# Kernel optimization log

Hardware: AMD Instinct MI355X
Metric: run time of the kernel (lower is better)

The kernel has to match this reference:

```python
import jax, jax.numpy as jnp
import numpy as np

N_NODES = 100000
N_EDGES = 1200000
D_IN = 64
D_HID = 64


def setup_inputs() -> dict:
    key = jax.random.key(0)
    k1, k2, k3, k4 = jax.random.split(key, 4)
    x = jax.random.normal(k1, (N_NODES, D_IN), dtype=jnp.float32)
    edge_index = jax.random.randint(k2, (2, N_EDGES), 0, N_NODES, dtype=jnp.int32)
    edge_attr = jax.random.uniform(k3, (N_EDGES,), dtype=jnp.float32)
    W = jax.random.normal(k4, (D_HID, D_IN), dtype=jnp.float32) / np.sqrt(D_IN)
    b = jnp.zeros((D_HID,), dtype=jnp.float32)
    return {"x": x, "edge_index": edge_index, "edge_attr": edge_attr, "W": W, "b": b}


def _gcn_conv(x, edge_index, edge_weight, W, b):
    # PyG GCNConv: add self-loops (weight 1), symmetric normalization,
    # linear transform, scatter-add aggregation at target (col), bias.
    n = x.shape[0]
    loop = jnp.arange(n, dtype=edge_index.dtype)
    row = jnp.concatenate([edge_index[0], loop])  # source
    col = jnp.concatenate([edge_index[1], loop])  # target
    ew = jnp.concatenate([edge_weight, jnp.ones((n,), edge_weight.dtype)])
    deg = jax.ops.segment_sum(ew, col, num_segments=n)  # [N]
    dis = jnp.where(deg > 0, jax.lax.rsqrt(deg), 0.0)
    norm = dis[row] * ew * dis[col]                     # [E+N]
    h = x @ W.T                                          # [N, D_HID]
    msg = norm[:, None] * h[row]                         # [E+N, D_HID]
    out = jax.ops.segment_sum(msg, col, num_segments=n)  # [N, D_HID]
    return out + b


def reference(x, edge_index, edge_attr, W, b):
    # layer_num=2 -> single GCNConv; dropout is identity in eval mode.
    h = _gcn_conv(x, edge_index, edge_attr, W, b)
    return jax.nn.relu(h)
```

## Files before the change

kernel.cpp:

```cpp
#include <hip/hip_runtime.h>

#define N_NODES 100000
#define N_EDGES 1200000
#define D 64
#define KP 68
#define TN 64
#define CAP 48
#define Q15 32767.0f
#define INVQ15 (1.0f / 32767.0f)
#define BW 512
#define BSH 9
#define NBKT ((N_NODES + BW - 1) / BW)
#define CAPB 8192

__device__ __forceinline__ unsigned short f2bf(float f) {
    unsigned u = __float_as_uint(f);
    return (unsigned short)((u + 0x7FFFu + ((u >> 16) & 1u)) >> 16);
}
__device__ __forceinline__ float bf2f(unsigned short h) {
    return __uint_as_float((unsigned)h << 16);
}

__global__ __launch_bounds__(256) void k_coarse(const int4* __restrict__ row4,
                                                const int4* __restrict__ col4,
                                                const float4* __restrict__ ew4,
                                                int* __restrict__ gcur,
                                                int2* __restrict__ coarse, int n4) {
    __shared__ int lcnt[NBKT];
    __shared__ int lbase[NBKT];
    int t = threadIdx.x;
    for (int i = t; i < NBKT; i += 256) lcnt[i] = 0;
    __syncthreads();

    int bkt[8]; int slot[8]; int2 rec[8];
    #pragma unroll
    for (int k = 0; k < 8; k++) bkt[k] = -1;

    #pragma unroll
    for (int r = 0; r < 2; r++) {
        int q = blockIdx.x * 512 + r * 256 + t;
        if (q < n4) {
            int4 rr = row4[q]; int4 cc = col4[q]; float4 ww = ew4[q];
            int j = r * 4;
            int c;
            c = cc.x; bkt[j+0] = c >> BSH;
            rec[j+0] = make_int2(rr.x, ((c & (BW-1)) << 15) | (int)(ww.x * Q15 + 0.5f));
            slot[j+0] = atomicAdd(&lcnt[bkt[j+0]], 1);
            c = cc.y; bkt[j+1] = c >> BSH;
            rec[j+1] = make_int2(rr.y, ((c & (BW-1)) << 15) | (int)(ww.y * Q15 + 0.5f));
            slot[j+1] = atomicAdd(&lcnt[bkt[j+1]], 1);
            c = cc.z; bkt[j+2] = c >> BSH;
            rec[j+2] = make_int2(rr.z, ((c & (BW-1)) << 15) | (int)(ww.z * Q15 + 0.5f));
            slot[j+2] = atomicAdd(&lcnt[bkt[j+2]], 1);
            c = cc.w; bkt[j+3] = c >> BSH;
            rec[j+3] = make_int2(rr.w, ((c & (BW-1)) << 15) | (int)(ww.w * Q15 + 0.5f));
            slot[j+3] = atomicAdd(&lcnt[bkt[j+3]], 1);
        }
    }
    __syncthreads();
    for (int i = t; i < NBKT; i += 256) lbase[i] = atomicAdd(&gcur[i], lcnt[i]);
    __syncthreads();
    #pragma unroll
    for (int k = 0; k < 8; k++) {
        if (bkt[k] >= 0) {
            int pos = lbase[bkt[k]] + slot[k];
            if (pos < CAPB) coarse[(size_t)bkt[k] * CAPB + pos] = rec[k];
        }
    }
}

__global__ __launch_bounds__(256) void k_bin(const int* __restrict__ gcur,
                                             const int2* __restrict__ coarse,
                                             int* __restrict__ cnt,
                                             float* __restrict__ dis,
                                             unsigned int* __restrict__ em, int n_nodes) {
    __shared__ int   cur512[BW];
    __shared__ float d512[BW];
    int b = blockIdx.x, t = threadIdx.x;
    int total = min(gcur[b], CAPB);
    int nbase = b * BW;
    int bw = min(BW, n_nodes - nbase);
    for (int i = t; i < BW; i += 256) { cur512[i] = 0; d512[i] = 0.f; }
    __syncthreads();
    const int2* src = &coarse[(size_t)b * CAPB];
    for (int i = t; i < total; i += 256) {
        int2 r = src[i];
        int cl = (r.y >> 15) & (BW - 1);
        float w = (float)(r.y & 0x7FFF) * INVQ15;
        int s = atomicAdd(&cur512[cl], 1);
        atomicAdd(&d512[cl], w);
        if (s < CAP)
            em[(size_t)(nbase + cl) * CAP + s] = ((unsigned)r.x << 15) | (unsigned)(r.y & 0x7FFF);
    }
    __syncthreads();
    for (int i = t; i < bw; i += 256) {
        cnt[nbase + i] = cur512[i];
        dis[nbase + i] = rsqrtf(1.0f + d512[i]);
    }
}

__global__ __launch_bounds__(256) void k_agg_cap(const int* __restrict__ cnt,
                                                 const unsigned int* __restrict__ em,
                                                 const unsigned short* __restrict__ hsb,
                                                 const float* __restrict__ dis,
                                                 const float* __restrict__ b,
                                                 float* __restrict__ out, int n_nodes) {
    int w = threadIdx.x >> 6, l = threadIdx.x & 63;
    int n = blockIdx.x * 4 + w;
    if (n >= n_nodes) return;
    int c = min(cnt[n], CAP);
    int recs = (int)em[(size_t)n * CAP + min(l, CAP - 1)];
    float acc = bf2f(hsb[(size_t)n * D + l]);

    int i = 0;
    for (; i + 8 <= c; i += 8) {
        unsigned r0 = (unsigned)__shfl(recs, i + 0);
        unsigned r1 = (unsigned)__shfl(recs, i + 1);
        unsigned r2 = (unsigned)__shfl(recs, i + 2);
        unsigned r3 = (unsigned)__shfl(recs, i + 3);
        unsigned r4 = (unsigned)__shfl(recs, i + 4);
        unsigned r5 = (unsigned)__shfl(recs, i + 5);
        unsigned r6 = (unsigned)__shfl(recs, i + 6);
        unsigned r7 = (unsigned)__shfl(recs, i + 7);
        float h0 = bf2f(hsb[(size_t)(r0 >> 15) * D + l]);
        float h1 = bf2f(hsb[(size_t)(r1 >> 15) * D + l]);
        float h2 = bf2f(hsb[(size_t)(r2 >> 15) * D + l]);
        float h3 = bf2f(hsb[(size_t)(r3 >> 15) * D + l]);
        float h4 = bf2f(hsb[(size_t)(r4 >> 15) * D + l]);
        float h5 = bf2f(hsb[(size_t)(r5 >> 15) * D + l]);
        float h6 = bf2f(hsb[(size_t)(r6 >> 15) * D + l]);
        float h7 = bf2f(hsb[(size_t)(r7 >> 15) * D + l]);
        acc = fmaf((float)(r0 & 0x7FFFu) * INVQ15, h0, acc);
        acc = fmaf((float)(r1 & 0x7FFFu) * INVQ15, h1, acc);
        acc = fmaf((float)(r2 & 0x7FFFu) * INVQ15, h2, acc);
        acc = fmaf((float)(r3 & 0x7FFFu) * INVQ15, h3, acc);
        acc = fmaf((float)(r4 & 0x7FFFu) * INVQ15, h4, acc);
        acc = fmaf((float)(r5 & 0x7FFFu) * INVQ15, h5, acc);
        acc = fmaf((float)(r6 & 0x7FFFu) * INVQ15, h6, acc);
        acc = fmaf((float)(r7 & 0x7FFFu) * INVQ15, h7, acc);
    }
    for (; i + 4 <= c; i += 4) {
        unsigned r0 = (unsigned)__shfl(recs, i + 0);
        unsigned r1 = (unsigned)__shfl(recs, i + 1);
        unsigned r2 = (unsigned)__shfl(recs, i + 2);
        unsigned r3 = (unsigned)__shfl(recs, i + 3);
        float h0 = bf2f(hsb[(size_t)(r0 >> 15) * D + l]);
        float h1 = bf2f(hsb[(size_t)(r1 >> 15) * D + l]);
        float h2 = bf2f(hsb[(size_t)(r2 >> 15) * D + l]);
        float h3 = bf2f(hsb[(size_t)(r3 >> 15) * D + l]);
        acc = fmaf((float)(r0 & 0x7FFFu) * INVQ15, h0, acc);
        acc = fmaf((float)(r1 & 0x7FFFu) * INVQ15, h1, acc);
        acc = fmaf((float)(r2 & 0x7FFFu) * INVQ15, h2, acc);
        acc = fmaf((float)(r3 & 0x7FFFu) * INVQ15, h3, acc);
    }
    for (; i < c; i++) {
        unsigned r = (unsigned)__shfl(recs, i);
        acc = fmaf((float)(r & 0x7FFFu) * INVQ15, bf2f(hsb[(size_t)(r >> 15) * D + l]), acc);
    }
    float v = fmaf(dis[n], acc, b[l]);
    out[(size_t)n * D + l] = v > 0.f ? v : 0.f;
}

__global__ __launch_bounds__(256) void k_gemm_tile(const float* __restrict__ x,
                                                   const float* __restrict__ W,
                                                   const float* __restrict__ dis,
                                                   unsigned short* __restrict__ hsb, int n_nodes) {
    __shared__ float wt[D * KP];
    int t = threadIdx.x;
    int base = blockIdx.x * TN;
    #pragma unroll
    for (int c = 0; c < 16; c++) {
        int idx = t + c * 256;
        wt[(idx & 63) * KP + (idx >> 6)] = W[idx];
    }
    __syncthreads();

    int tx = t & 15, ty = t >> 4;
    int f0 = tx * 4, n0 = base + ty * 4;
    const float* xr0 = x + (size_t)min(n0 + 0, n_nodes - 1) * D;
    const float* xr1 = x + (size_t)min(n0 + 1, n_nodes - 1) * D;
    const float* xr2 = x + (size_t)min(n0 + 2, n_nodes - 1) * D;
    const float* xr3 = x + (size_t)min(n0 + 3, n_nodes - 1) * D;

    float acc[4][4] = {};
    #pragma unroll 4
    for (int k = 0; k < D; k += 4) {
        float a[4][4], wv[4][4];
        *(float4*)a[0] = *(const float4*)&xr0[k];
        *(float4*)a[1] = *(const float4*)&xr1[k];
        *(float4*)a[2] = *(const float4*)&xr2[k];
        *(float4*)a[3] = *(const float4*)&xr3[k];
        #pragma unroll
        for (int kk = 0; kk < 4; kk++)
            *(float4*)wv[kk] = *(const float4*)&wt[(k + kk) * KP + f0];
        #pragma unroll
        for (int kk = 0; kk < 4; kk++)
            #pragma unroll
            for (int j = 0; j < 4; j++)
                #pragma unroll
                for (int ff = 0; ff < 4; ff++)
                    acc[j][ff] = fmaf(a[j][kk], wv[kk][ff], acc[j][ff]);
    }
    #pragma unroll
    for (int j = 0; j < 4; j++) {
        int n = n0 + j;
        if (n < n_nodes) {
            float dv = dis[n];
            unsigned short h0 = f2bf(dv * acc[j][0]);
            unsigned short h1 = f2bf(dv * acc[j][1]);
            unsigned short h2 = f2bf(dv * acc[j][2]);
            unsigned short h3 = f2bf(dv * acc[j][3]);
            uint2 pk;
            pk.x = (unsigned)h0 | ((unsigned)h1 << 16);
            pk.y = (unsigned)h2 | ((unsigned)h3 << 16);
            *(uint2*)&hsb[(size_t)n * D + f0] = pk;
        }
    }
}

extern "C" void kernel_launch(void* const* d_in, const int* in_sizes, int n_in,
                              void* d_out, int out_size, void* d_ws, size_t ws_size,
                              hipStream_t stream) {
    const float* x   = (const float*)d_in[0];
    const int*   ei  = (const int*)d_in[1];
    const float* ew  = (const float*)d_in[2];
    const float* W   = (const float*)d_in[3];
    const float* b   = (const float*)d_in[4];
    float* out = (float*)d_out;

    const int* row = ei;
    const int* col = ei + N_EDGES;

    char* p = (char*)d_ws;
    auto carve = [&](size_t bytes) { char* q = p; p += (bytes + 255) & ~(size_t)255; return q; };
    float*          dis    = (float*)carve(N_NODES * sizeof(float));
    unsigned short* hsb    = (unsigned short*)carve((size_t)N_NODES * D * sizeof(unsigned short));
    int*            cnt    = (int*)  carve(N_NODES * sizeof(int));
    unsigned int*   em     = (unsigned int*)carve((size_t)N_NODES * CAP * sizeof(unsigned int));
    int*            gcur   = (int*)  carve(NBKT * sizeof(int));
    int2*           coarse = (int2*) carve((size_t)NBKT * CAPB * sizeof(int2));

    hipMemsetAsync(gcur, 0, NBKT * sizeof(int), stream);

    int n4 = N_EDGES / 4;
    int nbA = (n4 + 511) / 512;
    k_coarse<<<nbA, 256, 0, stream>>>(
        (const int4*)row, (const int4*)col, (const float4*)ew, gcur, coarse, n4);
    k_bin<<<NBKT, 256, 0, stream>>>(gcur, coarse, cnt, dis, em, N_NODES);
    k_gemm_tile<<<(N_NODES + TN - 1) / TN, 256, 0, stream>>>(x, W, dis, hsb, N_NODES);
    k_agg_cap<<<(N_NODES + 3) / 4, 256, 0, stream>>>(cnt, em, hsb, dis, b, out, N_NODES);
}
```

Before: 172.4 us.

## Replace two-pass bucketed binning with direct packed 64-bit global atomics

Drops the coarse bucketing kernel and the per-bucket binning kernel. Each edge now does one 64-bit global atomicAdd on a per-node word that packs the slot count in the high bits and a fixed-point weight sum in the low bits, then writes its record straight into the target node's capped slot list. The degree normalisation is folded into the GEMM epilogue. This saves a launch and the coarse buffer round trip, at the cost of 1.2M scattered global atomics and scattered 4-byte stores instead of shared-memory atomics.

```diff
diff --git a/kernel.cpp b/kernel.cpp
--- a/kernel.cpp
+++ b/kernel.cpp
@@ -8,10 +8,9 @@
 #define CAP 48
 #define Q15 32767.0f
 #define INVQ15 (1.0f / 32767.0f)
-#define BW 512
-#define BSH 9
-#define NBKT ((N_NODES + BW - 1) / BW)
-#define CAPB 8192
+#define Q28 268435456.0f
+#define INVQ28 3.7252902984619140625e-09f
+#define CD_MASK ((1ULL << 40) - 1)
 
 __device__ __forceinline__ unsigned short f2bf(float f) {
     unsigned u = __float_as_uint(f);
@@ -21,85 +20,32 @@
     return __uint_as_float((unsigned)h << 16);
 }
 
-__global__ __launch_bounds__(256) void k_coarse(const int4* __restrict__ row4,
+__global__ __launch_bounds__(256) void k_direct(const int4* __restrict__ row4,
                                                 const int4* __restrict__ col4,
                                                 const float4* __restrict__ ew4,
-                                                int* __restrict__ gcur,
-                                                int2* __restrict__ coarse, int n4) {
-    __shared__ int lcnt[NBKT];
-    __shared__ int lbase[NBKT];
-    int t = threadIdx.x;
-    for (int i = t; i < NBKT; i += 256) lcnt[i] = 0;
-    __syncthreads();
+                                                unsigned long long* __restrict__ cd,
+                                                unsigned int* __restrict__ em, int n4) {
+    int q = blockIdx.x * 256 + threadIdx.x;
+    if (q >= n4) return;
+    int4 rr = row4[q];
+    int4 cc = col4[q];
+    float4 ww = ew4[q];
 
-    int bkt[8]; int slot[8]; int2 rec[8];
-    #pragma unroll
-    for (int k = 0; k < 8; k++) bkt[k] = -1;
-
-    #pragma unroll
-    for (int r = 0; r < 2; r++) {
-        int q = blockIdx.x * 512 + r * 256 + t;
-        if (q < n4) {
-            int4 rr = row4[q]; int4 cc = col4[q]; float4 ww = ew4[q];
-            int j = r * 4;
-            int c;
-            c = cc.x; bkt[j+0] = c >> BSH;
-            rec[j+0] = make_int2(rr.x, ((c & (BW-1)) << 15) | (int)(ww.x * Q15 + 0.5f));
-            slot[j+0] = atomicAdd(&lcnt[bkt[j+0]], 1);
-            c = cc.y; bkt[j+1] = c >> BSH;
-            rec[j+1] = make_int2(rr.y, ((c & (BW-1)) << 15) | (int)(ww.y * Q15 + 0.5f));
-            slot[j+1] = atomicAdd(&lcnt[bkt[j+1]], 1);
-            c = cc.z; bkt[j+2] = c >> BSH;
-            rec[j+2] = make_int2(rr.z, ((c & (BW-1)) << 15) | (int)(ww.z * Q15 + 0.5f));
-            slot[j+2] = atomicAdd(&lcnt[bkt[j+2]], 1);
-            c = cc.w; bkt[j+3] = c >> BSH;
-            rec[j+3] = make_int2(rr.w, ((c & (BW-1)) << 15) | (int)(ww.w * Q15 + 0.5f));
-            slot[j+3] = atomicAdd(&lcnt[bkt[j+3]], 1);
-        }
-    }
-    __syncthreads();
-    for (int i = t; i < NBKT; i += 256) lbase[i] = atomicAdd(&gcur[i], lcnt[i]);
-    __syncthreads();
-    #pragma unroll
-    for (int k = 0; k < 8; k++) {
-        if (bkt[k] >= 0) {
-            int pos = lbase[bkt[k]] + slot[k];
-            if (pos < CAPB) coarse[(size_t)bkt[k] * CAPB + pos] = rec[k];
-        }
-    }
+    unsigned long long o0 = atomicAdd(&cd[cc.x], (1ULL << 40) | (unsigned long long)(ww.x * Q28));
+    unsigned long long o1 = atomicAdd(&cd[cc.y], (1ULL << 40) | (unsigned long long)(ww.y * Q28));
+    unsigned long long o2 = atomicAdd(&cd[cc.z], (1ULL << 40) | (unsigned long long)(ww.z * Q28));
+    unsigned long long o3 = atomicAdd(&cd[cc.w], (1ULL << 40) | (unsigned long long)(ww.w * Q28));
+    int s0 = (int)(o0 >> 40);
+    int s1 = (int)(o1 >> 40);
+    int s2 = (int)(o2 >> 40);
+    int s3 = (int)(o3 >> 40);
+    if (s0 < CAP) em[(size_t)cc.x * CAP + s0] = ((unsigned)rr.x << 15) | (unsigned)(int)(ww.x * Q15 + 0.5f);
+    if (s1 < CAP) em[(size_t)cc.y * CAP + s1] = ((unsigned)rr.y << 15) | (unsigned)(int)(ww.y * Q15 + 0.5f);
+    if (s2 < CAP) em[(size_t)cc.z * CAP + s2] = ((unsigned)rr.z << 15) | (unsigned)(int)(ww.z * Q15 + 0.5f);
+    if (s3 < CAP) em[(size_t)cc.w * CAP + s3] = ((unsigned)rr.w << 15) | (unsigned)(int)(ww.w * Q15 + 0.5f);
 }
 
-__global__ __launch_bounds__(256) void k_bin(const int* __restrict__ gcur,
-                                             const int2* __restrict__ coarse,
-                                             int* __restrict__ cnt,
-                                             float* __restrict__ dis,
-                                             unsigned int* __restrict__ em, int n_nodes) {
-    __shared__ int   cur512[BW];
-    __shared__ float d512[BW];
-    int b = blockIdx.x, t = threadIdx.x;
-    int total = min(gcur[b], CAPB);
-    int nbase = b * BW;
-    int bw = min(BW, n_nodes - nbase);
-    for (int i = t; i < BW; i += 256) { cur512[i] = 0; d512[i] = 0.f; }
-    __syncthreads();
-    const int2* src = &coarse[(size_t)b * CAPB];
-    for (int i = t; i < total; i += 256) {
-        int2 r = src[i];
-        int cl = (r.y >> 15) & (BW - 1);
-        float w = (float)(r.y & 0x7FFF) * INVQ15;
-        int s = atomicAdd(&cur512[cl], 1);
-        atomicAdd(&d512[cl], w);
-        if (s < CAP)
-            em[(size_t)(nbase + cl) * CAP + s] = ((unsigned)r.x << 15) | (unsigned)(r.y & 0x7FFF);
-    }
-    __syncthreads();
-    for (int i = t; i < bw; i += 256) {
-        cnt[nbase + i] = cur512[i];
-        dis[nbase + i] = rsqrtf(1.0f + d512[i]);
-    }
-}
-
-__global__ __launch_bounds__(256) void k_agg_cap(const int* __restrict__ cnt,
+__global__ __launch_bounds__(256) void k_agg_cap(const unsigned long long* __restrict__ cd,
                                                  const unsigned int* __restrict__ em,
                                                  const unsigned short* __restrict__ hsb,
                                                  const float* __restrict__ dis,
@@ -108,7 +54,7 @@
     int w = threadIdx.x >> 6, l = threadIdx.x & 63;
     int n = blockIdx.x * 4 + w;
     if (n >= n_nodes) return;
-    int c = min(cnt[n], CAP);
+    int c = min((int)(cd[n] >> 40), CAP);
     int recs = (int)em[(size_t)n * CAP + min(l, CAP - 1)];
     float acc = bf2f(hsb[(size_t)n * D + l]);
 
@@ -163,7 +109,8 @@
 
 __global__ __launch_bounds__(256) void k_gemm_tile(const float* __restrict__ x,
                                                    const float* __restrict__ W,
-                                                   const float* __restrict__ dis,
+                                                   const unsigned long long* __restrict__ cd,
+                                                   float* __restrict__ dis,
                                                    unsigned short* __restrict__ hsb, int n_nodes) {
     __shared__ float wt[D * KP];
     int t = threadIdx.x;
@@ -205,7 +152,9 @@
     for (int j = 0; j < 4; j++) {
         int n = n0 + j;
         if (n < n_nodes) {
-            float dv = dis[n];
+            float wsum = (float)(cd[n] & CD_MASK) * INVQ28;
+            float dv = rsqrtf(1.0f + wsum);
+            dis[n] = dv;
             unsigned short h0 = f2bf(dv * acc[j][0]);
             unsigned short h1 = f2bf(dv * acc[j][1]);
             unsigned short h2 = f2bf(dv * acc[j][2]);
@@ -233,20 +182,17 @@
 
     char* p = (char*)d_ws;
     auto carve = [&](size_t bytes) { char* q = p; p += (bytes + 255) & ~(size_t)255; return q; };
-    float*          dis    = (float*)carve(N_NODES * sizeof(float));
-    unsigned short* hsb    = (unsigned short*)carve((size_t)N_NODES * D * sizeof(unsigned short));
-    int*            cnt    = (int*)  carve(N_NODES * sizeof(int));
-    unsigned int*   em     = (unsigned int*)carve((size_t)N_NODES * CAP * sizeof(unsigned int));
-    int*            gcur   = (int*)  carve(NBKT * sizeof(int));
-    int2*           coarse = (int2*) carve((size_t)NBKT * CAPB * sizeof(int2));
+    float*              dis = (float*)carve(N_NODES * sizeof(float));
+    unsigned short*     hsb = (unsigned short*)carve((size_t)N_NODES * D * sizeof(unsigned short));
+    unsigned long long* cd  = (unsigned long long*)carve(N_NODES * sizeof(unsigned long long));
+    unsigned int*       em  = (unsigned int*)carve((size_t)N_NODES * CAP * sizeof(unsigned int));
 
-    hipMemsetAsync(gcur, 0, NBKT * sizeof(int), stream);
+    hipMemsetAsync(cd, 0, N_NODES * sizeof(unsigned long long), stream);
 
     int n4 = N_EDGES / 4;
-    int nbA = (n4 + 511) / 512;
-    k_coarse<<<nbA, 256, 0, stream>>>(
-        (const int4*)row, (const int4*)col, (const float4*)ew, gcur, coarse, n4);
-    k_bin<<<NBKT, 256, 0, stream>>>(gcur, coarse, cnt, dis, em, N_NODES);
-    k_gemm_tile<<<(N_NODES + TN - 1) / TN, 256, 0, stream>>>(x, W, dis, hsb, N_NODES);
-    k_agg_cap<<<(N_NODES + 3) / 4, 256, 0, stream>>>(cnt, em, hsb, dis, b, out, N_NODES);
+    int nbA = (n4 + 255) / 256;
+    k_direct<<<nbA, 256, 0, stream>>>(
+        (const int4*)row, (const int4*)col, (const float4*)ew, cd, em, n4);
+    k_gemm_tile<<<(N_NODES + TN - 1) / TN, 256, 0, stream>>>(x, W, cd, dis, hsb, N_NODES);
+    k_agg_cap<<<(N_NODES + 3) / 4, 256, 0, stream>>>(cd, em, hsb, dis, b, out, N_NODES);
 }
```

New measurement: 234.9 us. 36.3% more time.

## Process two nodes per wavefront in aggregation, widen bin blocks, skip empty atomics

Applied to the files above, without the earlier changes.

The aggregation kernel now has each wavefront handle two destination nodes and interleave their 4-wide gather loops, so more independent gathers are in flight per wave. The binning kernel launches with 512 threads instead of 256 to work through each bucket faster. The coarse pass skips the global atomic for buckets with zero local count. The aggregation drops its bounds check and relies on the node count being divisible by 8. It also loses the 8-wide unroll, which may lower per-wave memory parallelism when degrees are uneven.

```diff
diff --git a/kernel.cpp b/kernel.cpp
--- a/kernel.cpp
+++ b/kernel.cpp
@@ -58,7 +58,10 @@
         }
     }
     __syncthreads();
-    for (int i = t; i < NBKT; i += 256) lbase[i] = atomicAdd(&gcur[i], lcnt[i]);
+    for (int i = t; i < NBKT; i += 256) {
+        int c = lcnt[i];
+        lbase[i] = c ? atomicAdd(&gcur[i], c) : 0;
+    }
     __syncthreads();
     #pragma unroll
     for (int k = 0; k < 8; k++) {
@@ -69,7 +72,7 @@
     }
 }
 
-__global__ __launch_bounds__(256) void k_bin(const int* __restrict__ gcur,
+__global__ __launch_bounds__(512) void k_bin(const int* __restrict__ gcur,
                                              const int2* __restrict__ coarse,
                                              int* __restrict__ cnt,
                                              float* __restrict__ dis,
@@ -80,10 +83,10 @@
     int total = min(gcur[b], CAPB);
     int nbase = b * BW;
     int bw = min(BW, n_nodes - nbase);
-    for (int i = t; i < BW; i += 256) { cur512[i] = 0; d512[i] = 0.f; }
+    for (int i = t; i < BW; i += 512) { cur512[i] = 0; d512[i] = 0.f; }
     __syncthreads();
     const int2* src = &coarse[(size_t)b * CAPB];
-    for (int i = t; i < total; i += 256) {
+    for (int i = t; i < total; i += 512) {
         int2 r = src[i];
         int cl = (r.y >> 15) & (BW - 1);
         float w = (float)(r.y & 0x7FFF) * INVQ15;
@@ -93,12 +96,17 @@
             em[(size_t)(nbase + cl) * CAP + s] = ((unsigned)r.x << 15) | (unsigned)(r.y & 0x7FFF);
     }
     __syncthreads();
-    for (int i = t; i < bw; i += 256) {
+    for (int i = t; i < bw; i += 512) {
         cnt[nbase + i] = cur512[i];
         dis[nbase + i] = rsqrtf(1.0f + d512[i]);
     }
 }
 
+#define AGG_STEP(rec, accv)                                                          \
+    {                                                                                \
+        float hh = bf2f(hsb[(size_t)((rec) >> 15) * D + l]);                         \
+        accv = fmaf((float)((rec) & 0x7FFFu) * INVQ15, hh, accv);                    \
+    }
 __global__ __launch_bounds__(256) void k_agg_cap(const int* __restrict__ cnt,
                                                  const unsigned int* __restrict__ em,
                                                  const unsigned short* __restrict__ hsb,
@@ -106,59 +114,85 @@
                                                  const float* __restrict__ b,
                                                  float* __restrict__ out, int n_nodes) {
     int w = threadIdx.x >> 6, l = threadIdx.x & 63;
-    int n = blockIdx.x * 4 + w;
-    if (n >= n_nodes) return;
-    int c = min(cnt[n], CAP);
-    int recs = (int)em[(size_t)n * CAP + min(l, CAP - 1)];
-    float acc = bf2f(hsb[(size_t)n * D + l]);
-
-    int i = 0;
-    for (; i + 8 <= c; i += 8) {
-        unsigned r0 = (unsigned)__shfl(recs, i + 0);
-        unsigned r1 = (unsigned)__shfl(recs, i + 1);
-        unsigned r2 = (unsigned)__shfl(recs, i + 2);
-        unsigned r3 = (unsigned)__shfl(recs, i + 3);
-        unsigned r4 = (unsigned)__shfl(recs, i + 4);
-        unsigned r5 = (unsigned)__shfl(recs, i + 5);
-        unsigned r6 = (unsigned)__shfl(recs, i + 6);
-        unsigned r7 = (unsigned)__shfl(recs, i + 7);
-        float h0 = bf2f(hsb[(size_t)(r0 >> 15) * D + l]);
-        float h1 = bf2f(hsb[(size_t)(r1 >> 15) * D + l]);
-        float h2 = bf2f(hsb[(size_t)(r2 >> 15) * D + l]);
-        float h3 = bf2f(hsb[(size_t)(r3 >> 15) * D + l]);
-        float h4 = bf2f(hsb[(size_t)(r4 >> 15) * D + l]);
-        float h5 = bf2f(hsb[(size_t)(r5 >> 15) * D + l]);
-        float h6 = bf2f(hsb[(size_t)(r6 >> 15) * D + l]);
-        float h7 = bf2f(hsb[(size_t)(r7 >> 15) * D + l]);
-        acc = fmaf((float)(r0 & 0x7FFFu) * INVQ15, h0, acc);
-        acc = fmaf((float)(r1 & 0x7FFFu) * INVQ15, h1, acc);
-        acc = fmaf((float)(r2 & 0x7FFFu) * INVQ15, h2, acc);
-        acc = fmaf((float)(r3 & 0x7FFFu) * INVQ15, h3, acc);
-        acc = fmaf((float)(r4 & 0x7FFFu) * INVQ15, h4, acc);
-        acc = fmaf((float)(r5 & 0x7FFFu) * INVQ15, h5, acc);
-        acc = fmaf((float)(r6 & 0x7FFFu) * INVQ15, h6, acc);
-        acc = fmaf((float)(r7 & 0x7FFFu) * INVQ15, h7, acc);
-    }
-    for (; i + 4 <= c; i += 4) {
-        unsigned r0 = (unsigned)__shfl(recs, i + 0);
-        unsigned r1 = (unsigned)__shfl(recs, i + 1);
-        unsigned r2 = (unsigned)__shfl(recs, i + 2);
-        unsigned r3 = (unsigned)__shfl(recs, i + 3);
-        float h0 = bf2f(hsb[(size_t)(r0 >> 15) * D + l]);
-        float h1 = bf2f(hsb[(size_t)(r1 >> 15) * D + l]);
-        float h2 = bf2f(hsb[(size_t)(r2 >> 15) * D + l]);
-        float h3 = bf2f(hsb[(size_t)(r3 >> 15) * D + l]);
-        acc = fmaf((float)(r0 & 0x7FFFu) * INVQ15, h0, acc);
-        acc = fmaf((float)(r1 & 0x7FFFu) * INVQ15, h1, acc);
-        acc = fmaf((float)(r2 & 0x7FFFu) * INVQ15, h2, acc);
-        acc = fmaf((float)(r3 & 0x7FFFu) * INVQ15, h3, acc);
-    }
-    for (; i < c; i++) {
-        unsigned r = (unsigned)__shfl(recs, i);
-        acc = fmaf((float)(r & 0x7FFFu) * INVQ15, bf2f(hsb[(size_t)(r >> 15) * D + l]), acc);
-    }
-    float v = fmaf(dis[n], acc, b[l]);
-    out[(size_t)n * D + l] = v > 0.f ? v : 0.f;
+    int n0 = blockIdx.x * 8 + w * 2;
+    int n1 = n0 + 1;
+    int c0 = min(cnt[n0], CAP);
+    int c1 = min(cnt[n1], CAP);
+    int recs0 = (int)em[(size_t)n0 * CAP + min(l, max(c0 - 1, 0))];
+    int recs1 = (int)em[(size_t)n1 * CAP + min(l, max(c1 - 1, 0))];
+    float acc0 = bf2f(hsb[(size_t)n0 * D + l]);
+    float acc1 = bf2f(hsb[(size_t)n1 * D + l]);
+
+    int i0 = 0, i1 = 0;
+    while (i0 + 4 <= c0 && i1 + 4 <= c1) {
+        unsigned a0 = (unsigned)__shfl(recs0, i0 + 0);
+        unsigned a1 = (unsigned)__shfl(recs0, i0 + 1);
+        unsigned a2 = (unsigned)__shfl(recs0, i0 + 2);
+        unsigned a3 = (unsigned)__shfl(recs0, i0 + 3);
+        unsigned b0 = (unsigned)__shfl(recs1, i1 + 0);
+        unsigned b1 = (unsigned)__shfl(recs1, i1 + 1);
+        unsigned b2 = (unsigned)__shfl(recs1, i1 + 2);
+        unsigned b3 = (unsigned)__shfl(recs1, i1 + 3);
+        float ha0 = bf2f(hsb[(size_t)(a0 >> 15) * D + l]);
+        float ha1 = bf2f(hsb[(size_t)(a1 >> 15) * D + l]);
+        float ha2 = bf2f(hsb[(size_t)(a2 >> 15) * D + l]);
+        float ha3 = bf2f(hsb[(size_t)(a3 >> 15) * D + l]);
+        float hb0 = bf2f(hsb[(size_t)(b0 >> 15) * D + l]);
+        float hb1 = bf2f(hsb[(size_t)(b1 >> 15) * D + l]);
+        float hb2 = bf2f(hsb[(size_t)(b2 >> 15) * D + l]);
+        float hb3 = bf2f(hsb[(size_t)(b3 >> 15) * D + l]);
+        acc0 = fmaf((float)(a0 & 0x7FFFu) * INVQ15, ha0, acc0);
+        acc0 = fmaf((float)(a1 & 0x7FFFu) * INVQ15, ha1, acc0);
+        acc0 = fmaf((float)(a2 & 0x7FFFu) * INVQ15, ha2, acc0);
+        acc0 = fmaf((float)(a3 & 0x7FFFu) * INVQ15, ha3, acc0);
+        acc1 = fmaf((float)(b0 & 0x7FFFu) * INVQ15, hb0, acc1);
+        acc1 = fmaf((float)(b1 & 0x7FFFu) * INVQ15, hb1, acc1);
+        acc1 = fmaf((float)(b2 & 0x7FFFu) * INVQ15, hb2, acc1);
+        acc1 = fmaf((float)(b3 & 0x7FFFu) * INVQ15, hb3, acc1);
+        i0 += 4; i1 += 4;
+    }
+    for (; i0 + 4 <= c0; i0 += 4) {
+        unsigned a0 = (unsigned)__shfl(recs0, i0 + 0);
+        unsigned a1 = (unsigned)__shfl(recs0, i0 + 1);
+        unsigned a2 = (unsigned)__shfl(recs0, i0 + 2);
+        unsigned a3 = (unsigned)__shfl(recs0, i0 + 3);
+        float ha0 = bf2f(hsb[(size_t)(a0 >> 15) * D + l]);
+        float ha1 = bf2f(hsb[(size_t)(a1 >> 15) * D + l]);
+        float ha2 = bf2f(hsb[(size_t)(a2 >> 15) * D + l]);
+        float ha3 = bf2f(hsb[(size_t)(a3 >> 15) * D + l]);
+        acc0 = fmaf((float)(a0 & 0x7FFFu) * INVQ15, ha0, acc0);
+        acc0 = fmaf((float)(a1 & 0x7FFFu) * INVQ15, ha1, acc0);
+        acc0 = fmaf((float)(a2 & 0x7FFFu) * INVQ15, ha2, acc0);
+        acc0 = fmaf((float)(a3 & 0x7FFFu) * INVQ15, ha3, acc0);
+    }
+    for (; i0 < c0; i0++) {
+        unsigned a = (unsigned)__shfl(recs0, i0);
+        AGG_STEP(a, acc0);
+    }
+    for (; i1 + 4 <= c1; i1 += 4) {
+        unsigned b0 = (unsigned)__shfl(recs1, i1 + 0);
+        unsigned b1 = (unsigned)__shfl(recs1, i1 + 1);
+        unsigned b2 = (unsigned)__shfl(recs1, i1 + 2);
+        unsigned b3 = (unsigned)__shfl(recs1, i1 + 3);
+        float hb0 = bf2f(hsb[(size_t)(b0 >> 15) * D + l]);
+        float hb1 = bf2f(hsb[(size_t)(b1 >> 15) * D + l]);
+        float hb2 = bf2f(hsb[(size_t)(b2 >> 15) * D + l]);
+        float hb3 = bf2f(hsb[(size_t)(b3 >> 15) * D + l]);
+        acc1 = fmaf((float)(b0 & 0x7FFFu) * INVQ15, hb0, acc1);
+        acc1 = fmaf((float)(b1 & 0x7FFFu) * INVQ15, hb1, acc1);
+        acc1 = fmaf((float)(b2 & 0x7FFFu) * INVQ15, hb2, acc1);
+        acc1 = fmaf((float)(b3 & 0x7FFFu) * INVQ15, hb3, acc1);
+    }
+    for (; i1 < c1; i1++) {
+        unsigned bb = (unsigned)__shfl(recs1, i1);
+        AGG_STEP(bb, acc1);
+    }
+
+    float bl = b[l];
+    float v0 = fmaf(dis[n0], acc0, bl);
+    float v1 = fmaf(dis[n1], acc1, bl);
+    out[(size_t)n0 * D + l] = v0 > 0.f ? v0 : 0.f;
+    out[(size_t)n1 * D + l] = v1 > 0.f ? v1 : 0.f;
 }
 
 __global__ __launch_bounds__(256) void k_gemm_tile(const float* __restrict__ x,
@@ -246,7 +280,7 @@
     int nbA = (n4 + 511) / 512;
     k_coarse<<<nbA, 256, 0, stream>>>(
         (const int4*)row, (const int4*)col, (const float4*)ew, gcur, coarse, n4);
-    k_bin<<<NBKT, 256, 0, stream>>>(gcur, coarse, cnt, dis, em, N_NODES);
+    k_bin<<<NBKT, 512, 0, stream>>>(gcur, coarse, cnt, dis, em, N_NODES);
     k_gemm_tile<<<(N_NODES + TN - 1) / TN, 256, 0, stream>>>(x, W, dis, hsb, N_NODES);
-    k_agg_cap<<<(N_NODES + 3) / 4, 256, 0, stream>>>(cnt, em, hsb, dis, b, out, N_NODES);
-}
+    k_agg_cap<<<N_NODES / 8, 256, 0, stream>>>(cnt, em, hsb, dis, b, out, N_NODES);
+}
```

Result: no change. 169.8 us (-1.5%).
